# Optimization experiments

Hardware: AMD Instinct MI355X
Metric: run time of the kernel (lower is better)

Reference implementation:

```python
import jax, jax.numpy as jnp
import numpy as np
from jax import lax

B, T = 8192, 128
HID = 64


def setup_inputs() -> dict:
    key = jax.random.key(0)
    ks = jax.random.split(key, 16)
    actor_ids = jax.random.randint(ks[0], (B, T), 0, 7, dtype=jnp.int32)
    action_ids = jax.random.randint(ks[1], (B, T), 0, 4, dtype=jnp.int32)
    street_ids = jax.random.randint(ks[2], (B, T), 0, 5, dtype=jnp.int32)
    bet_fraction = jax.random.uniform(ks[3], (B, T, 1), dtype=jnp.float32)
    # prefix-valid mask from random lengths (some zero-length rows)
    lengths = jax.random.randint(ks[4], (B,), 0, T + 1)
    valid_mask = jnp.arange(T)[None, :] < lengths[:, None]  # [B,T] bool
    s = 0.1
    params = {
        "E_actor": jax.random.normal(ks[5], (7, 8), jnp.float32) * s,
        "E_action": jax.random.normal(ks[6], (4, 8), jnp.float32) * s,
        "E_street": jax.random.normal(ks[7], (5, 4), jnp.float32) * s,
        "W_proj": jax.random.normal(ks[8], (32, 21), jnp.float32) * s,
        "b_proj": jax.random.normal(ks[9], (32,), jnp.float32) * s,
        "W_ih": jax.random.normal(ks[10], (3 * HID, 32), jnp.float32) * s,
        "W_hh": jax.random.normal(ks[11], (3 * HID, HID), jnp.float32) * s,
        "b_ih": jax.random.normal(ks[12], (3 * HID,), jnp.float32) * s,
        "b_hh": jax.random.normal(ks[13], (3 * HID,), jnp.float32) * s,
    }
    return dict(actor_ids=actor_ids, action_ids=action_ids, street_ids=street_ids,
                bet_fraction=bet_fraction, valid_mask=valid_mask, **params)


def reference(actor_ids, action_ids, street_ids, bet_fraction, valid_mask,
              E_actor, E_action, E_street, W_proj, b_proj,
              W_ih, W_hh, b_ih, b_hh):
    # embed + concat -> [B,T,21]
    feats = jnp.concatenate([E_actor[actor_ids], E_action[action_ids],
                             E_street[street_ids], bet_fraction], axis=-1)
    x = feats @ W_proj.T + b_proj                      # [B,T,32]
    # precompute input-side GRU gates for all timesteps: [B,T,3H]
    xg = x @ W_ih.T + b_ih
    xg_t = jnp.swapaxes(xg, 0, 1)                      # [T,B,3H]
    m_t = jnp.swapaxes(valid_mask, 0, 1)               # [T,B]

    def step(h, inp):
        xg_i, m = inp
        hg = h @ W_hh.T + b_hh                         # [B,3H]
        xr, xz, xn = jnp.split(xg_i, 3, axis=-1)
        hr, hz, hn = jnp.split(hg, 3, axis=-1)
        r = jax.nn.sigmoid(xr + hr)
        z = jax.nn.sigmoid(xz + hz)
        n = jnp.tanh(xn + r * hn)
        h_new = (1.0 - z) * n + z * h
        # only advance hidden state while t < length (prefix-valid mask);
        # final carry equals the GRU hidden at the last valid step, and rows
        # with length 0 stay at the zero init (matches torch masking).
        h = jnp.where(m[:, None], h_new, h)
        return h, None

    h0 = jnp.zeros((x.shape[0], HID), dtype=x.dtype)
    h_final, _ = lax.scan(step, h0, (xg_t, m_t))
    return h_final
```

## Files before the change

kernel.cpp:

```cpp
#include <hip/hip_runtime.h>

#define HID 64
#define TT  128
#define NROWS 8192
#define NGRP (NROWS / 16)
#define LOG2E 1.44269504088896f

typedef _Float16 half8 __attribute__((ext_vector_type(8)));
typedef float    f32x4 __attribute__((ext_vector_type(4)));


__global__ void k_len(const int* __restrict__ mask, int* __restrict__ lens) {
    const int row = blockIdx.x * 4 + (threadIdx.x >> 6);
    const int l   = threadIdx.x & 63;
    const int* mrow = mask + row * TT;
    int c = (mrow[l] != 0) + (mrow[l + 64] != 0);
    #pragma unroll
    for (int k = 32; k >= 1; k >>= 1) c += __shfl_xor(c, k);
    if (l == 0) lens[row] = c;
}

__global__ __launch_bounds__(1024) void k_sort(const int* __restrict__ lens,
                                               int* __restrict__ perm) {
    __shared__ int hist[TT + 1];
    __shared__ int offs[TT + 1];
    const int tid = threadIdx.x;
    if (tid <= TT) hist[tid] = 0;
    __syncthreads();
    int myL[8];
    #pragma unroll
    for (int i = 0; i < 8; i++) {
        myL[i] = lens[tid + 1024 * i];
        atomicAdd(&hist[myL[i]], 1);
    }
    __syncthreads();
    if (tid <= TT) {
        int s = 0;
        for (int j = 0; j < tid; j++) s += hist[j];
        offs[tid] = s;
    }
    __syncthreads();
    #pragma unroll
    for (int i = 0; i < 8; i++) {
        const int pos = atomicAdd(&offs[myL[i]], 1);
        const int d   = NROWS - 1 - pos;
        const int gd  = d >> 4, r = d & 15;
        const int b   = (gd < 256) ? gd : 767 - gd;
        perm[b * 16 + r] = tid + 1024 * i;
    }
}

__global__ __launch_bounds__(512, 4) void gru_fused(
    const int* __restrict__ actor_ids, const int* __restrict__ action_ids,
    const int* __restrict__ street_ids, const float* __restrict__ bet,
    const float* __restrict__ E_actor, const float* __restrict__ E_action,
    const float* __restrict__ E_street, const float* __restrict__ W_proj,
    const float* __restrict__ b_proj, const float* __restrict__ W_ih,
    const float* __restrict__ b_ih, const float* __restrict__ W_hh,
    const float* __restrict__ b_hh, const int* __restrict__ perm,
    const int* __restrict__ lens, float* __restrict__ out)
{
    __shared__ __align__(16) union {
        float wfs[192][32];
        struct {
            int pb[TT][17];
            __align__(16) _Float16 hb[2][16][72];
            int Lsh[16];
            int Psh[16];
        } c;
    } A;
    __shared__ __align__(16) _Float16 embl[144];
    __shared__ float bfs[192];

    const int tid  = threadIdx.x;
    const int wv   = tid >> 6;
    const int p    = wv >> 1;
    const int half = wv & 1;
    const int l    = tid & 63;
    const int q    = l >> 4;
    const int n    = l & 15;
    const int g    = blockIdx.x;

    for (int i = tid; i < 136; i += 512) {
        int r = i >> 3, m = i & 7;
        float v = 0.f;
        if (r < 7)       v = E_actor[r * 8 + m];
        else if (r < 11) v = E_action[(r - 7) * 8 + m];
        else if (r < 16) v = (m < 4) ? E_street[(r - 11) * 4 + m] : 0.f;
        embl[i] = (_Float16)v;
    }

    if (tid < 192) {
        const int j = tid;
        float wf[21];
        #pragma unroll
        for (int m = 0; m < 21; m++) wf[m] = 0.f;
        float bf = b_ih[j];
        for (int k = 0; k < 32; k++) {
            const float w = W_ih[j * 32 + k];
            bf += w * b_proj[k];
            #pragma unroll
            for (int m = 0; m < 21; m++) wf[m] += w * W_proj[k * 21 + m];
        }
        const float s = (j < 128) ? LOG2E : 2.f * LOG2E;
        #pragma unroll
        for (int m = 0; m < 21; m++) A.wfs[j][m] = wf[m] * s;
        #pragma unroll
        for (int m = 21; m < 32; m++) A.wfs[j][m] = 0.f;
        bfs[j] = bf;
    }
    __syncthreads();

    half8 Af[3], Ah[3][2];
    {
        const int m16 = l & 15, kq = l >> 4;
        #pragma unroll
        for (int g3 = 0; g3 < 3; g3++) {
            const int jr = g3 * 64 + p * 16 + m16;
            _Float16 v[8];
            #pragma unroll
            for (int m = 0; m < 8; m++) v[m] = (_Float16)A.wfs[jr][kq * 8 + m];
            Af[g3] = *(half8*)v;
            const float s = (g3 < 2) ? LOG2E : 2.f * LOG2E;
            #pragma unroll
            for (int kt = 0; kt < 2; kt++) {
                _Float16 w[8];
                #pragma unroll
                for (int m = 0; m < 8; m++)
                    w[m] = (_Float16)(W_hh[jr * HID + kt * 32 + kq * 8 + m] * s);
                Ah[g3][kt] = *(half8*)w;
            }
        }
    }
    f32x4 biasR, biasZ, biasX, biasH;
    #pragma unroll
    for (int e = 0; e < 4; e++) {
        const int idx = 16 * p + 4 * q + e;
        biasR[e] = (bfs[idx]      + b_hh[idx])      * LOG2E;
        biasZ[e] = (bfs[64 + idx] + b_hh[64 + idx]) * LOG2E;
        biasX[e] = bfs[128 + idx]  * (2.f * LOG2E);
        biasH[e] = b_hh[128 + idx] * (2.f * LOG2E);
    }
    __syncthreads();

    for (int i = tid; i < 2 * 16 * 72 / 2; i += 512) ((int*)A.c.hb)[i] = 0;
    {
        const int r = tid >> 5, tl = tid & 31;
        const int prow = perm[g * 16 + r];
        const int base = prow * TT;
        #pragma unroll
        for (int i = 0; i < 4; i++) {
            const int t = tl + 32 * i;
            const int a = actor_ids[base + t], c = action_ids[base + t];
            const int s = street_ids[base + t];
            const _Float16 f16 = (_Float16)bet[base + t];
            const unsigned fb = (unsigned)*(const unsigned short*)&f16;
            A.c.pb[t][r] = (int)(a | (c << 3) | (s << 5) | (fb << 16));
        }
        if (tl == 0) { A.c.Lsh[r] = lens[prow]; A.c.Psh[r] = prow; }
    }
    __syncthreads();

    const int Ln = A.c.Lsh[n];
    int Lmax = Ln;
    #pragma unroll
    for (int k = 1; k < 16; k <<= 1) {
        const int o = __shfl_xor(Lmax, k);
        Lmax = (o > Lmax) ? o : Lmax;
    }

    const bool isq2 = (q == 2);
    const int sh = (q == 1) ? 3 : (q == 2) ? 5 : 0;
    const int mk = (q == 1) ? 3 : (q == 3) ? 0 : 7;
    const int of = (q == 1) ? 7 : (q == 2) ? 11 : (q == 3) ? 16 : 0;

    const int j0 = 16 * p + 4 * q + 2 * half;
    float h0 = 0.f, h1 = 0.f;
    const f32x4 zero4 = {0.f, 0.f, 0.f, 0.f};

    f32x4 xR, xZ, xX;
    half8 Bfn;
    {
        const int p0 = A.c.pb[0][n];
        const int e0 = ((p0 >> sh) & mk) + of;
        half8 Bf0 = *(const half8*)&embl[e0 * 8];
        uint4* b0 = (uint4*)&Bf0;
        b0->z = isq2 ? ((unsigned)p0 >> 16) : b0->z;
        xR = __builtin_amdgcn_mfma_f32_16x16x32_f16(Af[0], Bf0, biasR, 0, 0, 0);
        xZ = __builtin_amdgcn_mfma_f32_16x16x32_f16(Af[1], Bf0, biasZ, 0, 0, 0);
        xX = __builtin_amdgcn_mfma_f32_16x16x32_f16(Af[2], Bf0, biasX, 0, 0, 0);

        const int p1 = A.c.pb[1][n];
        const int e1 = ((p1 >> sh) & mk) + of;
        half8 Bf1 = *(const half8*)&embl[e1 * 8];
        uint4* b1 = (uint4*)&Bf1;
        b1->z = isq2 ? ((unsigned)p1 >> 16) : b1->z;
        Bfn = Bf1;
    }

    for (int t = 0; t < Lmax; t++) {
        const int buf = t & 1;
        const half8 Bh0 = *(const half8*)&A.c.hb[buf][n][q * 8];
        const half8 Bh1 = *(const half8*)&A.c.hb[buf][n][32 + q * 8];
        const int t2 = (t + 2 < TT) ? t + 2 : TT - 1;
        const int p2 = A.c.pb[t2][n];

        f32x4 aRa = __builtin_amdgcn_mfma_f32_16x16x32_f16(Ah[0][0], Bh0, xR, 0, 0, 0);
        f32x4 aRb = __builtin_amdgcn_mfma_f32_16x16x32_f16(Ah[0][1], Bh1, zero4, 0, 0, 0);
        f32x4 aZ = __builtin_amdgcn_mfma_f32_16x16x32_f16(Ah[1][0], Bh0, xZ, 0, 0, 0);
        aZ = __builtin_amdgcn_mfma_f32_16x16x32_f16(Ah[1][1], Bh1, aZ, 0, 0, 0);
        f32x4 aH = __builtin_amdgcn_mfma_f32_16x16x32_f16(Ah[2][0], Bh0, biasH, 0, 0, 0);
        aH = __builtin_amdgcn_mfma_f32_16x16x32_f16(Ah[2][1], Bh1, aH, 0, 0, 0);
        const f32x4 aR = aRa + aRb;
        const f32x4 aXc = xX;

        const f32x4 xRn = __builtin_amdgcn_mfma_f32_16x16x32_f16(Af[0], Bfn, biasR, 0, 0, 0);
        const f32x4 xZn = __builtin_amdgcn_mfma_f32_16x16x32_f16(Af[1], Bfn, biasZ, 0, 0, 0);
        const f32x4 xXn = __builtin_amdgcn_mfma_f32_16x16x32_f16(Af[2], Bfn, biasX, 0, 0, 0);

        half8 Bf2;
        {
            const int e2 = ((p2 >> sh) & mk) + of;
            Bf2 = *(const half8*)&embl[e2 * 8];
            uint4* b2 = (uint4*)&Bf2;
            b2->z = isq2 ? ((unsigned)p2 >> 16) : b2->z;
        }

        const float vR0 = half ? aR[2]  : aR[0],  vR1 = half ? aR[3]  : aR[1];
        const float vZ0 = half ? aZ[2]  : aZ[0],  vZ1 = half ? aZ[3]  : aZ[1];
        const float vH0 = half ? aH[2]  : aH[0],  vH1 = half ? aH[3]  : aH[1];
        const float vX0 = half ? aXc[2] : aXc[0], vX1 = half ? aXc[3] : aXc[1];

        const bool live = (t < Ln);
        {
            const float r0 = __builtin_amdgcn_rcpf(1.f + __builtin_amdgcn_exp2f(-vR0));
            const float z0 = __builtin_amdgcn_rcpf(1.f + __builtin_amdgcn_exp2f(-vZ0));
            const float y0 = vX0 + r0 * vH0;
            const float n0 = 1.f - 2.f * __builtin_amdgcn_rcpf(1.f + __builtin_amdgcn_exp2f(y0));
            const float hv0 = n0 + z0 * (h0 - n0);
            h0 = live ? hv0 : h0;

            const float r1 = __builtin_amdgcn_rcpf(1.f + __builtin_amdgcn_exp2f(-vR1));
            const float z1 = __builtin_amdgcn_rcpf(1.f + __builtin_amdgcn_exp2f(-vZ1));
            const float y1 = vX1 + r1 * vH1;
            const float n1 = 1.f - 2.f * __builtin_amdgcn_rcpf(1.f + __builtin_amdgcn_exp2f(y1));
            const float hv1 = n1 + z1 * (h1 - n1);
            h1 = live ? hv1 : h1;
        }
        {
            const _Float16 a16 = (_Float16)h0, b16 = (_Float16)h1;
            const unsigned pk = (unsigned)*(const unsigned short*)&a16 |
                                ((unsigned)*(const unsigned short*)&b16 << 16);
            *(unsigned*)&A.c.hb[buf ^ 1][n][j0] = pk;
        }
        __syncthreads();

        xR = xRn; xZ = xZn; xX = xXn; Bfn = Bf2;
    }

    const int prow = A.c.Psh[n];
    *(float2*)&out[prow * HID + j0] = make_float2(h0, h1);
}

extern "C" void kernel_launch(void* const* d_in, const int* in_sizes, int n_in,
                              void* d_out, int out_size, void* d_ws, size_t ws_size,
                              hipStream_t stream) {
    const int*   actor_ids  = (const int*)d_in[0];
    const int*   action_ids = (const int*)d_in[1];
    const int*   street_ids = (const int*)d_in[2];
    const float* bet        = (const float*)d_in[3];
    const int*   vmask      = (const int*)d_in[4];
    const float* E_actor    = (const float*)d_in[5];
    const float* E_action   = (const float*)d_in[6];
    const float* E_street   = (const float*)d_in[7];
    const float* W_proj     = (const float*)d_in[8];
    const float* b_proj     = (const float*)d_in[9];
    const float* W_ih       = (const float*)d_in[10];
    const float* W_hh       = (const float*)d_in[11];
    const float* b_ih       = (const float*)d_in[12];
    const float* b_hh       = (const float*)d_in[13];
    float*       out        = (float*)d_out;

    int* ws   = (int*)d_ws;
    int* lens = ws;
    int* perm = ws + NROWS;

    k_len<<<NROWS / 4, 256, 0, stream>>>(vmask, lens);
    k_sort<<<1, 1024, 0, stream>>>(lens, perm);

    gru_fused<<<NGRP, 512, 0, stream>>>(actor_ids, action_ids, street_ids, bet,
                                        E_actor, E_action, E_street,
                                        W_proj, b_proj, W_ih, b_ih, W_hh, b_hh,
                                        perm, lens, out);
}
```

Before: 168.1 us.

## Shrink GRU row groups to 8 rows per 4-wave block

Each block now processes 8 length-sorted rows with 256 threads instead of 16 rows with 512. The row-duplicating wave pairs are replaced by duplicating the 8 rows across the 16 MFMA columns, with the `hf` bit choosing which outputs each lane keeps. The sort's permutation snakes across four stripes to spread long and short groups. Smaller groups should cut the padding from each block's Lmax and double the number of independent blocks. In exchange, half of every MFMA's column work is now redundant.

Measured after the change: 164.6 us. -2.1%, faster.

```diff
diff --git a/kernel.cpp b/kernel.cpp
--- a/kernel.cpp
+++ b/kernel.cpp
@@ -3,7 +3,7 @@
 #define HID 64
 #define TT  128
 #define NROWS 8192
-#define NGRP (NROWS / 16)
+#define NGRP (NROWS / 8)
 #define LOG2E 1.44269504088896f
 
 typedef _Float16 half8 __attribute__((ext_vector_type(8)));
@@ -44,13 +44,17 @@
     for (int i = 0; i < 8; i++) {
         const int pos = atomicAdd(&offs[myL[i]], 1);
         const int d   = NROWS - 1 - pos;
-        const int gd  = d >> 4, r = d & 15;
-        const int b   = (gd < 256) ? gd : 767 - gd;
-        perm[b * 16 + r] = tid + 1024 * i;
-    }
-}
-
-__global__ __launch_bounds__(512, 4) void gru_fused(
+        const int g8  = d >> 3, r = d & 7;
+        int b;
+        if      (g8 < 256) b = g8;
+        else if (g8 < 512) b = 256 + (511 - g8);
+        else if (g8 < 768) b = 512 + (g8 - 512);
+        else               b = 768 + (1023 - g8);
+        perm[b * 8 + r] = tid + 1024 * i;
+    }
+}
+
+__global__ __launch_bounds__(256, 4) void gru_fused(
     const int* __restrict__ actor_ids, const int* __restrict__ action_ids,
     const int* __restrict__ street_ids, const float* __restrict__ bet,
     const float* __restrict__ E_actor, const float* __restrict__ E_action,
@@ -63,25 +67,25 @@
     __shared__ __align__(16) union {
         float wfs[192][32];
         struct {
-            int pb[TT][17];
-            __align__(16) _Float16 hb[2][16][72];
-            int Lsh[16];
-            int Psh[16];
+            int pb[TT][9];
+            __align__(16) _Float16 hb[2][8][72];
+            int Lsh[8];
+            int Psh[8];
         } c;
     } A;
     __shared__ __align__(16) _Float16 embl[144];
     __shared__ float bfs[192];
 
-    const int tid  = threadIdx.x;
-    const int wv   = tid >> 6;
-    const int p    = wv >> 1;
-    const int half = wv & 1;
-    const int l    = tid & 63;
-    const int q    = l >> 4;
-    const int n    = l & 15;
-    const int g    = blockIdx.x;
-
-    for (int i = tid; i < 136; i += 512) {
+    const int tid = threadIdx.x;
+    const int wv  = tid >> 6;
+    const int l   = tid & 63;
+    const int q   = l >> 4;
+    const int cc  = l & 15;
+    const int cr  = cc & 7;
+    const int hf  = cc >> 3;
+    const int g   = blockIdx.x;
+
+    for (int i = tid; i < 136; i += 256) {
         int r = i >> 3, m = i & 7;
         float v = 0.f;
         if (r < 7)       v = E_actor[r * 8 + m];
@@ -116,7 +120,7 @@
         const int m16 = l & 15, kq = l >> 4;
         #pragma unroll
         for (int g3 = 0; g3 < 3; g3++) {
-            const int jr = g3 * 64 + p * 16 + m16;
+            const int jr = g3 * 64 + wv * 16 + m16;
             _Float16 v[8];
             #pragma unroll
             for (int m = 0; m < 8; m++) v[m] = (_Float16)A.wfs[jr][kq * 8 + m];
@@ -135,7 +139,7 @@
     f32x4 biasR, biasZ, biasX, biasH;
     #pragma unroll
     for (int e = 0; e < 4; e++) {
-        const int idx = 16 * p + 4 * q + e;
+        const int idx = 16 * wv + 4 * q + e;
         biasR[e] = (bfs[idx]      + b_hh[idx])      * LOG2E;
         biasZ[e] = (bfs[64 + idx] + b_hh[64 + idx]) * LOG2E;
         biasX[e] = bfs[128 + idx]  * (2.f * LOG2E);
@@ -143,10 +147,10 @@
     }
     __syncthreads();
 
-    for (int i = tid; i < 2 * 16 * 72 / 2; i += 512) ((int*)A.c.hb)[i] = 0;
+    for (int i = tid; i < 2 * 8 * 72 / 2; i += 256) ((int*)A.c.hb)[i] = 0;
     {
         const int r = tid >> 5, tl = tid & 31;
-        const int prow = perm[g * 16 + r];
+        const int prow = perm[g * 8 + r];
         const int base = prow * TT;
         #pragma unroll
         for (int i = 0; i < 4; i++) {
@@ -161,27 +165,25 @@
     }
     __syncthreads();
 
-    const int Ln = A.c.Lsh[n];
+    const int Ln = A.c.Lsh[cr];
     int Lmax = Ln;
-    #pragma unroll
-    for (int k = 1; k < 16; k <<= 1) {
-        const int o = __shfl_xor(Lmax, k);
-        Lmax = (o > Lmax) ? o : Lmax;
-    }
+    { int o = __shfl_xor(Lmax, 1); Lmax = o > Lmax ? o : Lmax; }
+    { int o = __shfl_xor(Lmax, 2); Lmax = o > Lmax ? o : Lmax; }
+    { int o = __shfl_xor(Lmax, 4); Lmax = o > Lmax ? o : Lmax; }
 
     const bool isq2 = (q == 2);
     const int sh = (q == 1) ? 3 : (q == 2) ? 5 : 0;
     const int mk = (q == 1) ? 3 : (q == 3) ? 0 : 7;
     const int of = (q == 1) ? 7 : (q == 2) ? 11 : (q == 3) ? 16 : 0;
 
-    const int j0 = 16 * p + 4 * q + 2 * half;
+    const int j0 = 16 * wv + 4 * q + 2 * hf;
     float h0 = 0.f, h1 = 0.f;
     const f32x4 zero4 = {0.f, 0.f, 0.f, 0.f};
 
     f32x4 xR, xZ, xX;
     half8 Bfn;
     {
-        const int p0 = A.c.pb[0][n];
+        const int p0 = A.c.pb[0][cr];
         const int e0 = ((p0 >> sh) & mk) + of;
         half8 Bf0 = *(const half8*)&embl[e0 * 8];
         uint4* b0 = (uint4*)&Bf0;
@@ -190,7 +192,7 @@
         xZ = __builtin_amdgcn_mfma_f32_16x16x32_f16(Af[1], Bf0, biasZ, 0, 0, 0);
         xX = __builtin_amdgcn_mfma_f32_16x16x32_f16(Af[2], Bf0, biasX, 0, 0, 0);
 
-        const int p1 = A.c.pb[1][n];
+        const int p1 = A.c.pb[1][cr];
         const int e1 = ((p1 >> sh) & mk) + of;
         half8 Bf1 = *(const half8*)&embl[e1 * 8];
         uint4* b1 = (uint4*)&Bf1;
@@ -200,10 +202,10 @@
 
     for (int t = 0; t < Lmax; t++) {
         const int buf = t & 1;
-        const half8 Bh0 = *(const half8*)&A.c.hb[buf][n][q * 8];
-        const half8 Bh1 = *(const half8*)&A.c.hb[buf][n][32 + q * 8];
+        const half8 Bh0 = *(const half8*)&A.c.hb[buf][cr][q * 8];
+        const half8 Bh1 = *(const half8*)&A.c.hb[buf][cr][32 + q * 8];
         const int t2 = (t + 2 < TT) ? t + 2 : TT - 1;
-        const int p2 = A.c.pb[t2][n];
+        const int p2 = A.c.pb[t2][cr];
 
         f32x4 aRa = __builtin_amdgcn_mfma_f32_16x16x32_f16(Ah[0][0], Bh0, xR, 0, 0, 0);
         f32x4 aRb = __builtin_amdgcn_mfma_f32_16x16x32_f16(Ah[0][1], Bh1, zero4, 0, 0, 0);
@@ -226,10 +228,10 @@
             b2->z = isq2 ? ((unsigned)p2 >> 16) : b2->z;
         }
 
-        const float vR0 = half ? aR[2]  : aR[0],  vR1 = half ? aR[3]  : aR[1];
-        const float vZ0 = half ? aZ[2]  : aZ[0],  vZ1 = half ? aZ[3]  : aZ[1];
-        const float vH0 = half ? aH[2]  : aH[0],  vH1 = half ? aH[3]  : aH[1];
-        const float vX0 = half ? aXc[2] : aXc[0], vX1 = half ? aXc[3] : aXc[1];
+        const float vR0 = hf ? aR[2]  : aR[0],  vR1 = hf ? aR[3]  : aR[1];
+        const float vZ0 = hf ? aZ[2]  : aZ[0],  vZ1 = hf ? aZ[3]  : aZ[1];
+        const float vH0 = hf ? aH[2]  : aH[0],  vH1 = hf ? aH[3]  : aH[1];
+        const float vX0 = hf ? aXc[2] : aXc[0], vX1 = hf ? aXc[3] : aXc[1];
 
         const bool live = (t < Ln);
         {
@@ -251,14 +253,14 @@
             const _Float16 a16 = (_Float16)h0, b16 = (_Float16)h1;
             const unsigned pk = (unsigned)*(const unsigned short*)&a16 |
                                 ((unsigned)*(const unsigned short*)&b16 << 16);
-            *(unsigned*)&A.c.hb[buf ^ 1][n][j0] = pk;
+            *(unsigned*)&A.c.hb[buf ^ 1][cr][j0] = pk;
         }
         __syncthreads();
 
         xR = xRn; xZ = xZn; xX = xXn; Bfn = Bf2;
     }
 
-    const int prow = A.c.Psh[n];
+    const int prow = A.c.Psh[cr];
     *(float2*)&out[prow * HID + j0] = make_float2(h0, h1);
 }
 
@@ -288,7 +290,7 @@
     k_len<<<NROWS / 4, 256, 0, stream>>>(vmask, lens);
     k_sort<<<1, 1024, 0, stream>>>(lens, perm);
 
-    gru_fused<<<NGRP, 512, 0, stream>>>(actor_ids, action_ids, street_ids, bet,
+    gru_fused<<<NGRP, 256, 0, stream>>>(actor_ids, action_ids, street_ids, bet,
                                         E_actor, E_action, E_street,
                                         W_proj, b_proj, W_ih, b_ih, W_hh, b_hh,
                                         perm, lens, out);
```
